# Performance work log

Measured on AMD Instinct MI355X. Metric: run time of the kernel, lower is better.

The kernel has to match this reference:

```python
import jax, jax.numpy as jnp
import numpy as np

N_HEAD = 8
D_HEAD = 64  # emb_size == d_model // n_head


def _proj(x, w):
    # x: (B, 1, d_model, max_len), w: (n_head*emb_size, 1, 25, 1) -> conv VALID
    y = jax.lax.conv_general_dilated(
        x, w, window_strides=(1, 1), padding='VALID',
        dimension_numbers=('NCHW', 'OIHW', 'NCHW'))  # (B, C, H1, L)
    B, C, H1, L = y.shape
    y = y.reshape(B, C, H1 // N_HEAD, N_HEAD, L).mean(axis=3)  # (B, C, H2, L)
    # view(B, -1, n_head, d_head).transpose(1, 2) -> (B, n_head, S, d_head)
    y = y.reshape(B, -1, N_HEAD, D_HEAD).transpose(0, 2, 1, 3)
    return y


def setup_inputs() -> dict:
    key = jax.random.key(0)
    ks = jax.random.split(key, 7)
    B, d_model, max_len = 8, 512, 16
    C = N_HEAD * D_HEAD  # 512
    return {
        'query': jax.random.normal(ks[0], (B, 1, d_model, max_len), jnp.float32),
        'key':   jax.random.normal(ks[1], (B, 1, d_model, max_len), jnp.float32),
        'value': jax.random.normal(ks[2], (B, 1, d_model, max_len), jnp.float32),
        'wq': jax.random.normal(ks[3], (C, 1, 25, 1), jnp.float32) * 0.1,
        'wk': jax.random.normal(ks[4], (C, 1, 25, 1), jnp.float32) * 0.1,
        'wv': jax.random.normal(ks[5], (C, 1, 25, 1), jnp.float32) * 0.1,
        'w_out': jax.random.normal(ks[6], (1, 1, 1, 1), jnp.float32),
        'b_out': jnp.zeros((1,), jnp.float32),
    }


def reference(query, key, value, wq, wk, wv, w_out, b_out):
    q = _proj(query, wq)   # (B, H, S, Dh)
    k = _proj(key, wk)
    v = _proj(value, wv)
    scale = 1.0 / jnp.sqrt(jnp.asarray(D_HEAD, q.dtype))
    scores = jnp.einsum('bhqd,bhkd->bhqk', q, k) * scale
    attn = jax.nn.softmax(scores, axis=-1)  # dropout is identity in eval
    x = jnp.einsum('bhqk,bhkd->bhqd', attn, v)
    B = x.shape[0]
    x = x.transpose(0, 2, 1, 3).reshape(B, -1, N_HEAD * D_HEAD)  # (B, S, d_model)
    # conv_out: 1x1 Conv2d(1,1) == scalar scale + bias
    x = x * w_out.reshape(()) + b_out.reshape(())
    return x, attn
```

## Files before the change

kernel.cpp:

```cpp
#include <hip/hip_runtime.h>
#include <hip/hip_bf16.h>
#include <cstdint>
#include <cstddef>

#define B_    8
#define H_    8
#define BH_   64
#define S_    976
#define SP_   992
#define D_    64
#define DM_   512
#define L_    16
#define H2_   61
#define KW_   25
#define EFF_  32
#define XOFF  3997696
#define OSTR  68
#define PWR   492
#define TFL   15616

typedef __attribute__((ext_vector_type(8))) short bf16x8;
typedef __attribute__((ext_vector_type(4))) short bf16x4;
typedef __attribute__((ext_vector_type(4))) unsigned short u16x4;
typedef __attribute__((ext_vector_type(4))) float f32x4;

__device__ __forceinline__ unsigned short f2bfu(float f) {
    union { float f; unsigned u; } v; v.f = f;
    unsigned u = v.u;
    u += 0x7fffu + ((u >> 16) & 1u);
    return (unsigned short)(u >> 16);
}
__device__ __forceinline__ unsigned packbf(float a, float b) {
    return (unsigned)f2bfu(a) | ((unsigned)f2bfu(b) << 16);
}
__device__ __forceinline__ float bflo(unsigned u) {
    union { unsigned u; float f; } v; v.u = u << 16; return v.f;
}
__device__ __forceinline__ float bfhi(unsigned u) {
    union { unsigned u; float f; } v; v.u = u & 0xffff0000u; return v.f;
}

__device__ __forceinline__ f32x4 mfma16(bf16x4 a, bf16x4 b, f32x4 c) {
#if __has_builtin(__builtin_amdgcn_mfma_f32_16x16x16bf16_1k)
    return __builtin_amdgcn_mfma_f32_16x16x16bf16_1k(a, b, c, 0, 0, 0);
#else
    asm volatile("v_mfma_f32_16x16x16_bf16 %0, %1, %2, %0"
                 : "+v"(c) : "v"(a), "v"(b));
    return c;
#endif
}

__global__ __launch_bounds__(256) void proj_kernel(
    const float* __restrict__ qin, const float* __restrict__ kin,
    const float* __restrict__ vin, const float* __restrict__ wq,
    const float* __restrict__ wk, const float* __restrict__ wv,
    short* __restrict__ qws, short* __restrict__ kws, short* __restrict__ vtws) {
    __shared__ float xl[536 * L_];
    __shared__ float wl[32 * 32];
    int blk = blockIdx.x;
    int cg  = blk & 15;
    int b   = (blk >> 4) & 7;
    int tz  = blk >> 7;
    const float* x    = (tz == 0) ? qin : (tz == 1) ? kin : vin;
    const float* wsrc = (tz == 0) ? wq  : (tz == 1) ? wk  : wv;

    const float4* xb4 = (const float4*)(x + b * DM_ * L_);
    float4* xl4 = (float4*)xl;
    for (int i = threadIdx.x; i < DM_ * L_ / 4; i += 256) xl4[i] = xb4[i];
    for (int i = DM_ * L_ + threadIdx.x; i < 536 * L_; i += 256) xl[i] = 0.f;

    for (int i = threadIdx.x; i < 1024; i += 256) {
        int ci = i >> 5;
        int t  = i & 31;
        int c  = cg * 32 + ci;
        int jlo = (t - 24 > 0) ? t - 24 : 0;
        int jhi = (t < 7) ? t : 7;
        float s = 0.f;
        for (int jj = jlo; jj <= jhi; ++jj) s += wsrc[c * KW_ + (t - jj)];
        wl[i] = s * 0.125f;
    }
    __syncthreads();

    int c_local = threadIdx.x >> 3;
    int slot    = threadIdx.x & 7;
    int c       = cg * 32 + c_local;
    float wreg[EFF_];
    #pragma unroll
    for (int i = 0; i < EFF_; ++i) wreg[i] = wl[c_local * 32 + i];

    for (int it = 0; it < 8; ++it) {
        int pt  = slot + it * 8;
        int h2b = pt >> 2;
        int l0  = (pt & 3) * 4;
        float acc[4][4];
        #pragma unroll
        for (int d = 0; d < 4; ++d)
            #pragma unroll
            for (int jj = 0; jj < 4; ++jj) acc[d][jj] = 0.f;
        const float* xp = &xl[(h2b * 32) * L_ + l0];
        #pragma unroll
        for (int k = 0; k < 56; ++k) {
            float4 xv = *(const float4*)(xp + k * L_);
            #pragma unroll
            for (int d = 0; d < 4; ++d) {
                int t = k - 8 * d;
                if (t >= 0 && t < EFF_) {
                    acc[d][0] = fmaf(xv.x, wreg[t], acc[d][0]);
                    acc[d][1] = fmaf(xv.y, wreg[t], acc[d][1]);
                    acc[d][2] = fmaf(xv.z, wreg[t], acc[d][2]);
                    acc[d][3] = fmaf(xv.w, wreg[t], acc[d][3]);
                }
            }
        }
        #pragma unroll
        for (int d = 0; d < 4; ++d) {
            int h2 = h2b * 4 + d;
            if (h2 < H2_) {
                int f0   = c * S_ + h2 * L_ + l0;
                int s    = f0 >> 9;
                int head = (f0 >> 6) & 7;
                int dh   = f0 & 63;
                int bh   = b * H_ + head;
                if (tz == 2) {
                    #pragma unroll
                    for (int jj = 0; jj < 4; ++jj)
                        vtws[((size_t)bh * D_ + dh + jj) * SP_ + s] =
                            (short)f2bfu(acc[d][jj]);
                } else {
                    u16x4 u = { f2bfu(acc[d][0]), f2bfu(acc[d][1]),
                                f2bfu(acc[d][2]), f2bfu(acc[d][3]) };
                    short* dst = (tz == 0) ? qws : kws;
                    *(u16x4*)(void*)&dst[((size_t)bh * S_ + s) * D_ + dh] = u;
                }
            }
        }
    }
}

__global__ __launch_bounds__(256) void attn_kernel(
    const short* __restrict__ qws, const short* __restrict__ kws,
    const short* __restrict__ vtws, const float* __restrict__ w_out,
    const float* __restrict__ b_out, float* __restrict__ out) {
    __shared__ unsigned pw[16][PWR];
    __shared__ float sums[4][16];
    __shared__ float inv16[16];

    int w    = threadIdx.x >> 6;
    int lane = threadIdx.x & 63;
    int l16  = lane & 15;
    int g    = lane >> 4;

    int blk = blockIdx.x;
    int xcd = blk & 7;
    int j   = blk >> 3;
    int bh  = xcd + 8 * (j / H2_);
    int qt  = j % H2_;
    int s0  = qt * 16;

    int t0 = (w == 0) ? 0 : 16 + (w - 1) * 15;
    int nt = (w == 0) ? 16 : 15;

    const short* qb = qws + ((size_t)bh * S_ + s0 + l16) * D_ + g * 8;
    bf16x8 q0 = *(const bf16x8*)qb;
    bf16x8 q1 = *(const bf16x8*)(qb + 32);
    const short* kbase = kws + ((size_t)bh * S_ + l16) * D_ + g * 8;
    const short* vbase = vtws + ((size_t)bh * D_ + l16) * SP_ + g * 4;

    f32x4 o0 = {0.f,0.f,0.f,0.f}, o1 = {0.f,0.f,0.f,0.f};
    f32x4 o2 = {0.f,0.f,0.f,0.f}, o3 = {0.f,0.f,0.f,0.f};
    float sa = 0.f, sb = 0.f, sc_ = 0.f, sd = 0.f;

    #pragma unroll
    for (int ct = 0; ct < 16; ++ct) {
        if (ct < nt) {
            int gt = t0 + ct;
            const short* kb = kbase + (size_t)gt * 16 * D_;
            bf16x8 k0 = *(const bf16x8*)kb;
            bf16x8 k1 = *(const bf16x8*)(kb + 32);
            const short* vb = vbase + gt * 16;
            bf16x4 v0 = *(const bf16x4*)(vb);
            bf16x4 v1 = *(const bf16x4*)(vb + 16 * SP_);
            bf16x4 v2 = *(const bf16x4*)(vb + 32 * SP_);
            bf16x4 v3 = *(const bf16x4*)(vb + 48 * SP_);
            f32x4 acc = {0.f, 0.f, 0.f, 0.f};
            acc = __builtin_amdgcn_mfma_f32_16x16x32_bf16(k0, q0, acc, 0, 0, 0);
            acc = __builtin_amdgcn_mfma_f32_16x16x32_bf16(k1, q1, acc, 0, 0, 0);
            float e0 = __expf(acc[0] * 0.125f);
            float e1 = __expf(acc[1] * 0.125f);
            float e2 = __expf(acc[2] * 0.125f);
            float e3 = __expf(acc[3] * 0.125f);
            sa += e0; sb += e1; sc_ += e2; sd += e3;
            unsigned u0 = packbf(e0, e1);
            unsigned u1 = packbf(e2, e3);
            uint2 pk2 = {u0, u1};
            *(uint2*)(void*)&pw[l16][gt * 8 + g * 2] = pk2;
            union { uint2 u; bf16x4 v; } pc;
            pc.u.x = u0; pc.u.y = u1;
            o0 = mfma16(pc.v, v0, o0);
            o1 = mfma16(pc.v, v1, o1);
            o2 = mfma16(pc.v, v2, o2);
            o3 = mfma16(pc.v, v3, o3);
        }
    }
    float sum = (sa + sb) + (sc_ + sd);
    sum += __shfl_xor(sum, 16);
    sum += __shfl_xor(sum, 32);
    if (lane < 16) sums[w][l16] = sum;
    __syncthreads();

    if (threadIdx.x < 16) {
        int r = threadIdx.x;
        inv16[r] = 1.f / ((sums[0][r] + sums[1][r]) +
                          (sums[2][r] + sums[3][r]));
    }
    __syncthreads();

    {
        float* tbase = out + XOFF + ((size_t)bh * S_ + s0) * S_;
        int base = w * 256 + lane * 4;
        #pragma unroll
        for (int rd = 0; rd < 16; ++rd) {
            int ff = rd * 1024 + base;
            if (ff < TFL) {
                int r = ((ff >> 4) * 2149) >> 17;
                int c = ff - 976 * r;
                uint2 raw = *(const uint2*)(void*)&pw[r][c >> 1];
                float invr = inv16[r];
                f32x4 pv = { bflo(raw.x) * invr, bfhi(raw.x) * invr,
                             bflo(raw.y) * invr, bfhi(raw.y) * invr };
                *(f32x4*)(tbase + ff) = pv;
            }
        }
    }
    __syncthreads();

    float* olds = (float*)&pw[0][0];
    {
        float* ob = olds + w * 16 * OSTR;
        #pragma unroll
        for (int i = 0; i < 4; ++i) {
            int q = g * 4 + i;
            ob[q * OSTR +  0 + l16] = o0[i];
            ob[q * OSTR + 16 + l16] = o1[i];
            ob[q * OSTR + 32 + l16] = o2[i];
            ob[q * OSTR + 48 + l16] = o3[i];
        }
    }
    __syncthreads();

    {
        float wo = w_out[0], bo = b_out[0];
        int b = bh >> 3, hh = bh & 7;
        #pragma unroll
        for (int rr = 0; rr < 4; ++rr) {
            int r = w * 4 + rr;
            float s1 = inv16[r] * wo;
            int o = r * OSTR + lane;
            float v = olds[o] + olds[16*OSTR + o] + olds[32*OSTR + o] +
                      olds[48*OSTR + o];
            out[((size_t)b * S_ + s0 + r) * DM_ + hh * D_ + lane] = v * s1 + bo;
        }
    }
}

extern "C" void kernel_launch(void* const* d_in, const int* in_sizes, int n_in,
                              void* d_out, int out_size, void* d_ws, size_t ws_size,
                              hipStream_t stream) {
    const float* q   = (const float*)d_in[0];
    const float* k   = (const float*)d_in[1];
    const float* v   = (const float*)d_in[2];
    const float* wq  = (const float*)d_in[3];
    const float* wk  = (const float*)d_in[4];
    const float* wv  = (const float*)d_in[5];
    const float* wo  = (const float*)d_in[6];
    const float* bo  = (const float*)d_in[7];

    char* ws = (char*)d_ws;
    short* qws  = (short*)(ws + 196608);
    short* kws  = qws + (size_t)BH_ * S_ * D_;
    short* vtws = kws + (size_t)BH_ * S_ * D_;

    proj_kernel<<<384, 256, 0, stream>>>(q, k, v, wq, wk, wv, qws, kws, vtws);
    attn_kernel<<<BH_ * H2_, 256, 0, stream>>>(qws, kws, vtws, wo, bo,
                                               (float*)d_out);
}
```

Before: 178.0 us.

## Split projection across more blocks and write attention probs directly from registers

The projection kernel is split four ways along the pooled-row axis, so it launches four times as many blocks, each staging only a 152-row slice of the input in LDS. The attention kernel drops the large LDS probability buffer. Each lane now keeps its packed bf16 probabilities in registers and writes normalized rows straight to global memory with nontemporal stores. Work is split evenly at 16 tiles per wave, with the out-of-range tile clamped and masked, which adds some wasted MFMA work but removes the LDS round trip and one barrier.

```diff
diff --git a/kernel.cpp b/kernel.cpp
--- a/kernel.cpp
+++ b/kernel.cpp
@@ -16,8 +16,6 @@
 #define EFF_  32
 #define XOFF  3997696
 #define OSTR  68
-#define PWR   492
-#define TFL   15616
 
 typedef __attribute__((ext_vector_type(8))) short bf16x8;
 typedef __attribute__((ext_vector_type(4))) short bf16x4;
@@ -55,20 +53,24 @@
     const float* __restrict__ vin, const float* __restrict__ wq,
     const float* __restrict__ wk, const float* __restrict__ wv,
     short* __restrict__ qws, short* __restrict__ kws, short* __restrict__ vtws) {
-    __shared__ float xl[536 * L_];
+    __shared__ float xl[152 * L_];
     __shared__ float wl[32 * 32];
     int blk = blockIdx.x;
     int cg  = blk & 15;
     int b   = (blk >> 4) & 7;
-    int tz  = blk >> 7;
+    int q4  = (blk >> 7) & 3;
+    int tz  = blk >> 9;
     const float* x    = (tz == 0) ? qin : (tz == 1) ? kin : vin;
     const float* wsrc = (tz == 0) ? wq  : (tz == 1) ? wk  : wv;
 
+    int r0 = 128 * q4;
     const float4* xb4 = (const float4*)(x + b * DM_ * L_);
     float4* xl4 = (float4*)xl;
-    for (int i = threadIdx.x; i < DM_ * L_ / 4; i += 256) xl4[i] = xb4[i];
-    for (int i = DM_ * L_ + threadIdx.x; i < 536 * L_; i += 256) xl[i] = 0.f;
-
+    float4 z4 = {0.f, 0.f, 0.f, 0.f};
+    for (int i = threadIdx.x; i < 152 * 4; i += 256) {
+        int gi = r0 * 4 + i;
+        xl4[i] = (gi < DM_ * 4) ? xb4[gi] : z4;
+    }
     for (int i = threadIdx.x; i < 1024; i += 256) {
         int ci = i >> 5;
         int t  = i & 31;
@@ -88,16 +90,19 @@
     #pragma unroll
     for (int i = 0; i < EFF_; ++i) wreg[i] = wl[c_local * 32 + i];
 
-    for (int it = 0; it < 8; ++it) {
-        int pt  = slot + it * 8;
-        int h2b = pt >> 2;
-        int l0  = (pt & 3) * 4;
+    #pragma unroll
+    for (int itl = 0; itl < 2; ++itl) {
+        int it    = q4 * 2 + itl;
+        int pt    = slot + it * 8;
+        int h2b   = pt >> 2;
+        int h2b_l = (slot + 8 * itl) >> 2;
+        int l0    = (pt & 3) * 4;
         float acc[4][4];
         #pragma unroll
         for (int d = 0; d < 4; ++d)
             #pragma unroll
             for (int jj = 0; jj < 4; ++jj) acc[d][jj] = 0.f;
-        const float* xp = &xl[(h2b * 32) * L_ + l0];
+        const float* xp = &xl[(h2b_l * 32) * L_ + l0];
         #pragma unroll
         for (int k = 0; k < 56; ++k) {
             float4 xv = *(const float4*)(xp + k * L_);
@@ -141,7 +146,7 @@
     const short* __restrict__ qws, const short* __restrict__ kws,
     const short* __restrict__ vtws, const float* __restrict__ w_out,
     const float* __restrict__ b_out, float* __restrict__ out) {
-    __shared__ unsigned pw[16][PWR];
+    __shared__ float olds[4][16 * OSTR];
     __shared__ float sums[4][16];
     __shared__ float inv16[16];
 
@@ -157,8 +162,7 @@
     int qt  = j % H2_;
     int s0  = qt * 16;
 
-    int t0 = (w == 0) ? 0 : 16 + (w - 1) * 15;
-    int nt = (w == 0) ? 16 : 15;
+    int t0 = w * 16;
 
     const short* qb = qws + ((size_t)bh * S_ + s0 + l16) * D_ + g * 8;
     bf16x8 q0 = *(const bf16x8*)qb;
@@ -166,48 +170,48 @@
     const short* kbase = kws + ((size_t)bh * S_ + l16) * D_ + g * 8;
     const short* vbase = vtws + ((size_t)bh * D_ + l16) * SP_ + g * 4;
 
+    unsigned pp[16][2];
     f32x4 o0 = {0.f,0.f,0.f,0.f}, o1 = {0.f,0.f,0.f,0.f};
     f32x4 o2 = {0.f,0.f,0.f,0.f}, o3 = {0.f,0.f,0.f,0.f};
     float sa = 0.f, sb = 0.f, sc_ = 0.f, sd = 0.f;
 
     #pragma unroll
     for (int ct = 0; ct < 16; ++ct) {
-        if (ct < nt) {
-            int gt = t0 + ct;
-            const short* kb = kbase + (size_t)gt * 16 * D_;
-            bf16x8 k0 = *(const bf16x8*)kb;
-            bf16x8 k1 = *(const bf16x8*)(kb + 32);
-            const short* vb = vbase + gt * 16;
-            bf16x4 v0 = *(const bf16x4*)(vb);
-            bf16x4 v1 = *(const bf16x4*)(vb + 16 * SP_);
-            bf16x4 v2 = *(const bf16x4*)(vb + 32 * SP_);
-            bf16x4 v3 = *(const bf16x4*)(vb + 48 * SP_);
-            f32x4 acc = {0.f, 0.f, 0.f, 0.f};
-            acc = __builtin_amdgcn_mfma_f32_16x16x32_bf16(k0, q0, acc, 0, 0, 0);
-            acc = __builtin_amdgcn_mfma_f32_16x16x32_bf16(k1, q1, acc, 0, 0, 0);
-            float e0 = __expf(acc[0] * 0.125f);
-            float e1 = __expf(acc[1] * 0.125f);
-            float e2 = __expf(acc[2] * 0.125f);
-            float e3 = __expf(acc[3] * 0.125f);
-            sa += e0; sb += e1; sc_ += e2; sd += e3;
-            unsigned u0 = packbf(e0, e1);
-            unsigned u1 = packbf(e2, e3);
-            uint2 pk2 = {u0, u1};
-            *(uint2*)(void*)&pw[l16][gt * 8 + g * 2] = pk2;
-            union { uint2 u; bf16x4 v; } pc;
-            pc.u.x = u0; pc.u.y = u1;
-            o0 = mfma16(pc.v, v0, o0);
-            o1 = mfma16(pc.v, v1, o1);
-            o2 = mfma16(pc.v, v2, o2);
-            o3 = mfma16(pc.v, v3, o3);
-        }
+        int gt  = t0 + ct;
+        int gtc = (gt > 60) ? 60 : gt;
+        const short* kb = kbase + (size_t)gtc * 16 * D_;
+        bf16x8 k0 = *(const bf16x8*)kb;
+        bf16x8 k1 = *(const bf16x8*)(kb + 32);
+        const short* vb = vbase + gtc * 16;
+        bf16x4 v0 = *(const bf16x4*)(vb);
+        bf16x4 v1 = *(const bf16x4*)(vb + 16 * SP_);
+        bf16x4 v2 = *(const bf16x4*)(vb + 32 * SP_);
+        bf16x4 v3 = *(const bf16x4*)(vb + 48 * SP_);
+        f32x4 acc = {0.f, 0.f, 0.f, 0.f};
+        acc = __builtin_amdgcn_mfma_f32_16x16x32_bf16(k0, q0, acc, 0, 0, 0);
+        acc = __builtin_amdgcn_mfma_f32_16x16x32_bf16(k1, q1, acc, 0, 0, 0);
+        bool live = (gt <= 60);
+        float e0 = live ? __expf(acc[0] * 0.125f) : 0.f;
+        float e1 = live ? __expf(acc[1] * 0.125f) : 0.f;
+        float e2 = live ? __expf(acc[2] * 0.125f) : 0.f;
+        float e3 = live ? __expf(acc[3] * 0.125f) : 0.f;
+        sa += e0; sb += e1; sc_ += e2; sd += e3;
+        unsigned u0 = packbf(e0, e1);
+        unsigned u1 = packbf(e2, e3);
+        pp[ct][0] = u0;
+        pp[ct][1] = u1;
+        union { uint2 u; bf16x4 v; } pc;
+        pc.u.x = u0; pc.u.y = u1;
+        o0 = mfma16(pc.v, v0, o0);
+        o1 = mfma16(pc.v, v1, o1);
+        o2 = mfma16(pc.v, v2, o2);
+        o3 = mfma16(pc.v, v3, o3);
     }
     float sum = (sa + sb) + (sc_ + sd);
     sum += __shfl_xor(sum, 16);
     sum += __shfl_xor(sum, 32);
     if (lane < 16) sums[w][l16] = sum;
     __syncthreads();
-
     if (threadIdx.x < 16) {
         int r = threadIdx.x;
         inv16[r] = 1.f / ((sums[0][r] + sums[1][r]) +
@@ -216,27 +220,23 @@
     __syncthreads();
 
     {
-        float* tbase = out + XOFF + ((size_t)bh * S_ + s0) * S_;
-        int base = w * 256 + lane * 4;
-        #pragma unroll
-        for (int rd = 0; rd < 16; ++rd) {
-            int ff = rd * 1024 + base;
-            if (ff < TFL) {
-                int r = ((ff >> 4) * 2149) >> 17;
-                int c = ff - 976 * r;
-                uint2 raw = *(const uint2*)(void*)&pw[r][c >> 1];
-                float invr = inv16[r];
-                f32x4 pv = { bflo(raw.x) * invr, bfhi(raw.x) * invr,
-                             bflo(raw.y) * invr, bfhi(raw.y) * invr };
-                *(f32x4*)(tbase + ff) = pv;
+        float invr = inv16[l16];
+        float* arow = out + XOFF + ((size_t)bh * S_ + s0 + l16) * S_;
+        #pragma unroll
+        for (int ct = 0; ct < 16; ++ct) {
+            int gt = t0 + ct;
+            if (gt <= 60) {
+                unsigned u0 = pp[ct][0], u1 = pp[ct][1];
+                f32x4 pv = { bflo(u0) * invr, bfhi(u0) * invr,
+                             bflo(u1) * invr, bfhi(u1) * invr };
+                __builtin_nontemporal_store(pv,
+                    (f32x4*)(arow + gt * 16 + g * 4));
             }
         }
     }
-    __syncthreads();
-
-    float* olds = (float*)&pw[0][0];
+
     {
-        float* ob = olds + w * 16 * OSTR;
+        float* ob = &olds[w][0];
         #pragma unroll
         for (int i = 0; i < 4; ++i) {
             int q = g * 4 + i;
@@ -256,8 +256,7 @@
             int r = w * 4 + rr;
             float s1 = inv16[r] * wo;
             int o = r * OSTR + lane;
-            float v = olds[o] + olds[16*OSTR + o] + olds[32*OSTR + o] +
-                      olds[48*OSTR + o];
+            float v = olds[0][o] + olds[1][o] + olds[2][o] + olds[3][o];
             out[((size_t)b * S_ + s0 + r) * DM_ + hh * D_ + lane] = v * s1 + bo;
         }
     }
@@ -280,7 +279,7 @@
     short* kws  = qws + (size_t)BH_ * S_ * D_;
     short* vtws = kws + (size_t)BH_ * S_ * D_;
 
-    proj_kernel<<<384, 256, 0, stream>>>(q, k, v, wq, wk, wv, qws, kws, vtws);
+    proj_kernel<<<1536, 256, 0, stream>>>(q, k, v, wq, wk, wv, qws, kws, vtws);
     attn_kernel<<<BH_ * H2_, 256, 0, stream>>>(qws, kws, vtws, wo, bo,
                                                (float*)d_out);
 }
```

After: 215.7 us. +21.2%, slower.
